# Kernel tuning notes

Measured on AMD Instinct MI355X. Metric: run time of the kernel, lower is better.

The kernel has to match this reference:

```python
import jax, jax.numpy as jnp
import numpy as np

B, O, R = 4, 1000, 20000
NF, RD, ED = 6, 1, 100
RH, OH = 150, 100


def setup_inputs() -> dict:
    key = jax.random.key(0)
    ks = jax.random.split(key, 20)
    s = 0.05
    inp = {
        "objects": jax.random.normal(ks[0], (B, O, NF), jnp.float32),
        "sender_relations": jax.random.uniform(ks[1], (B, O, R), jnp.float32),
        "receiver_relations": jax.random.uniform(ks[2], (B, O, R), jnp.float32),
        "relation_info": jax.random.normal(ks[3], (B, R, RD), jnp.float32),
        # relational MLP: (2*NF+RD) -> 150 -> 150 -> 150 -> ED, ReLU after every layer
        "rw1": jax.random.normal(ks[4], (2 * NF + RD, RH), jnp.float32) * s,
        "rb1": jnp.zeros((RH,), jnp.float32),
        "rw2": jax.random.normal(ks[5], (RH, RH), jnp.float32) * s,
        "rb2": jnp.zeros((RH,), jnp.float32),
        "rw3": jax.random.normal(ks[6], (RH, RH), jnp.float32) * s,
        "rb3": jnp.zeros((RH,), jnp.float32),
        "rw4": jax.random.normal(ks[7], (RH, ED), jnp.float32) * s,
        "rb4": jnp.zeros((ED,), jnp.float32),
        # object MLP: (NF+ED) -> 100 -> 2, ReLU only after first layer
        "ow1": jax.random.normal(ks[8], (NF + ED, OH), jnp.float32) * s,
        "ob1": jnp.zeros((OH,), jnp.float32),
        "ow2": jax.random.normal(ks[9], (OH, 2), jnp.float32) * s,
        "ob2": jnp.zeros((2,), jnp.float32),
    }
    return inp


def reference(objects, sender_relations, receiver_relations, relation_info,
              rw1, rb1, rw2, rb2, rw3, rb3, rw4, rb4,
              ow1, ob1, ow2, ob2):
    # marshalling: dense one-hot gather via bmm
    senders = jnp.einsum('bnr,bnf->brf', sender_relations, objects)    # [B,R,NF]
    receivers = jnp.einsum('bnr,bnf->brf', receiver_relations, objects)  # [B,R,NF]
    Bm = jnp.concatenate([senders, receivers, relation_info], axis=2)  # [B,R,2NF+RD]
    # relational MLP (ReLU after every layer, including the last)
    h = jax.nn.relu(Bm @ rw1 + rb1)
    h = jax.nn.relu(h @ rw2 + rb2)
    h = jax.nn.relu(h @ rw3 + rb3)
    E = jax.nn.relu(h @ rw4 + rb4)                                     # [B,R,ED]
    # aggregator: dense scatter via bmm
    effect_receivers = jnp.einsum('bnr,brf->bnf', receiver_relations, E)  # [B,O,ED]
    C = jnp.concatenate([objects, effect_receivers], axis=2)           # [B,O,NF+ED]
    # object MLP, flattened over batch*objects like the torch view(-1, input)
    Cf = C.reshape(-1, C.shape[-1])
    o = jax.nn.relu(Cf @ ow1 + ob1)
    return o @ ow2 + ob2                                               # [B*O, 2]
```

## Files before the change

kernel.cpp:

```cpp
#include <hip/hip_runtime.h>

#define B_   4
#define O_   1000
#define R_   20000
#define NF_  6
#define EDP_ 128
#define KS_  25
#define CHUNK_ 800
#define MPAD_ 1024

#define ET_OFF   2560000
#define PART_OFF 7680000
#define WT_USHORTS (4 * 2 * 25600)

typedef short bf16x8 __attribute__((ext_vector_type(8)));
typedef float f32x4  __attribute__((ext_vector_type(4)));
typedef unsigned short ushort4v __attribute__((ext_vector_type(4)));
typedef unsigned short ushort8v __attribute__((ext_vector_type(8)));

#define MFMA16 __builtin_amdgcn_mfma_f32_16x16x32_bf16

__device__ __forceinline__ unsigned short f2bf(float x) {
    union { float f; unsigned int u; } v; v.f = x;
    unsigned int r = (v.u + 0x7FFFu + ((v.u >> 16) & 1u)) >> 16;
    return (unsigned short)r;
}

__device__ __forceinline__ float bf2f(unsigned short h) {
    union { unsigned int u; float f; } v; v.u = (unsigned int)h << 16;
    return v.f;
}

__global__ __launch_bounds__(256) void k_prep(
    const float* __restrict__ rw1, const float* __restrict__ rb1,
    const float* __restrict__ rw2, const float* __restrict__ rb2,
    const float* __restrict__ rw3, const float* __restrict__ rb3,
    const float* __restrict__ rw4, const float* __restrict__ rb4,
    unsigned short* __restrict__ Wt, float* __restrict__ bfp)
{
    const int l = blockIdx.y;
    const float* Ws[4] = {rw1, rw2, rw3, rw4};
    const float* Bs[4] = {rb1, rb2, rb3, rb4};
    const int   Ksz[4] = {13, 150, 150, 150};
    const int   Nsz[4] = {150, 150, 150, 100};
    const float* w = Ws[l];
    const int K = Ksz[l], N = Nsz[l];

    int idx = blockIdx.x * 256 + threadIdx.x;
    if (idx < 25600) {
        int n = idx / 160, k = idx % 160;
        float v = (k < K && n < N) ? w[k * N + n] : 0.f;
        unsigned short h = f2bf(v);
        unsigned short lo = f2bf(v - bf2f(h));
        Wt[(size_t)l * 51200 + idx]         = h;
        Wt[(size_t)l * 51200 + 25600 + idx] = lo;
    }
    if (blockIdx.x == 0 && threadIdx.x < 160)
        bfp[l * 160 + threadIdx.x] = (threadIdx.x < (unsigned)N) ? Bs[l][threadIdx.x] : 0.f;
}

__global__ __launch_bounds__(256) void k_marshal(
    const float* __restrict__ obj, const float* __restrict__ S,
    const float* __restrict__ RRm, const float* __restrict__ rinfo,
    float* __restrict__ bmp)
{
    __shared__ float sobj[500 * NF_];
    const int b = blockIdx.y, z = blockIdx.z;
    const int n0 = z * 500;
    for (int i = threadIdx.x; i < 500 * NF_; i += 256)
        sobj[i] = obj[(size_t)b * O_ * NF_ + (size_t)n0 * NF_ + i];
    __syncthreads();

    const int r = blockIdx.x * 256 + threadIdx.x;
    if (r >= R_) return;

    const size_t base = (size_t)b * O_ * R_ + (size_t)n0 * R_ + r;
    const float* Sp = S + base;
    const float* Rp = RRm + base;

    float ss[NF_] = {0.f, 0.f, 0.f, 0.f, 0.f, 0.f};
    float rs[NF_] = {0.f, 0.f, 0.f, 0.f, 0.f, 0.f};

    #pragma unroll 4
    for (int n = 0; n < 500; ++n) {
        float sv = Sp[(size_t)n * R_];
        float rv = Rp[(size_t)n * R_];
        #pragma unroll
        for (int f = 0; f < NF_; ++f) {
            float o = sobj[n * NF_ + f];
            ss[f] = fmaf(sv, o, ss[f]);
            rs[f] = fmaf(rv, o, rs[f]);
        }
    }

    float* outp = bmp + ((size_t)z * 80000 + (size_t)b * R_ + r) * 16;
    #pragma unroll
    for (int f = 0; f < NF_; ++f) {
        outp[f]     = ss[f];
        outp[6 + f] = rs[f];
    }
    outp[12] = (z == 0) ? rinfo[(size_t)b * R_ + r] : 0.f;
}

template<int NT>
__device__ __forceinline__ void layer_mm2(
    const unsigned short (*act)[168],
    const unsigned short* __restrict__ Wh, const unsigned short* __restrict__ Wl,
    int arow0, int koff, int cl, f32x4 (*acc)[10])
{
    #pragma unroll
    for (int m = 0; m < 2; ++m)
        #pragma unroll
        for (int n = 0; n < NT; ++n) acc[m][n] = (f32x4){0.f, 0.f, 0.f, 0.f};
    #pragma unroll
    for (int ks = 0; ks < 5; ++ks) {
        bf16x8 a0 = *(const bf16x8*)&act[arow0][ks * 32 + koff];
        bf16x8 a1 = *(const bf16x8*)&act[arow0 + 16][ks * 32 + koff];
        #pragma unroll
        for (int n = 0; n < NT; ++n) {
            bf16x8 wh = *(const bf16x8*)(Wh + (size_t)(n * 16 + cl) * 160 + ks * 32 + koff);
            bf16x8 wl = *(const bf16x8*)(Wl + (size_t)(n * 16 + cl) * 160 + ks * 32 + koff);
            acc[0][n] = MFMA16(a0, wh, acc[0][n], 0, 0, 0);
            acc[0][n] = MFMA16(a0, wl, acc[0][n], 0, 0, 0);
            acc[1][n] = MFMA16(a1, wh, acc[1][n], 0, 0, 0);
            acc[1][n] = MFMA16(a1, wl, acc[1][n], 0, 0, 0);
        }
    }
}

template<int NT>
__device__ __forceinline__ void epi2(
    f32x4 (*acc)[10], const float* __restrict__ bias,
    unsigned short (*out)[168], int m0, int cl, int rg0)
{
    __syncthreads();
    #pragma unroll
    for (int m = 0; m < 2; ++m) {
        #pragma unroll
        for (int n = 0; n < NT; ++n) {
            int col = n * 16 + cl;
            float bv = bias[col];
            #pragma unroll
            for (int rg = 0; rg < 4; ++rg) {
                float v = fmaxf(acc[m][n][rg] + bv, 0.f);
                out[m0 + m * 16 + rg0 + rg][col] = f2bf(v);
            }
        }
    }
    __syncthreads();
}

__global__ __launch_bounds__(256) void k_mlp(
    const float* __restrict__ bmp, unsigned short* __restrict__ Et,
    const unsigned short* __restrict__ Wt, const float* __restrict__ bfp)
{
    __shared__ unsigned short act[128][168];
    __shared__ unsigned short alo[128][32];
    const int t = threadIdx.x;
    const size_t row0 = (size_t)blockIdx.x * 128;

    for (int idx = t; idx < 128 * 32; idx += 256) {
        int rr = idx >> 5, k = idx & 31;
        float v = 0.f;
        if (k < 13)
            v = bmp[(row0 + rr) * 16 + k]
              + bmp[(size_t)80000 * 16 + (row0 + rr) * 16 + k];
        unsigned short h = f2bf(v);
        act[rr][k] = h;
        alo[rr][k] = f2bf(v - bf2f(h));
    }
    __syncthreads();

    const int lane = t & 63, wave = t >> 6;
    const int m0    = wave * 32;
    const int arow0 = m0 + (lane & 15);
    const int koff  = (lane >> 4) * 8;
    const int cl    = lane & 15;
    const int rg0   = (lane >> 4) * 4;

    f32x4 acc[2][10];

    {
        const unsigned short* Wh = Wt;
        const unsigned short* Wl = Wt + 25600;
        bf16x8 ah0 = *(const bf16x8*)&act[arow0][koff];
        bf16x8 al0 = *(const bf16x8*)&alo[arow0][koff];
        bf16x8 ah1 = *(const bf16x8*)&act[arow0 + 16][koff];
        bf16x8 al1 = *(const bf16x8*)&alo[arow0 + 16][koff];
        #pragma unroll
        for (int n = 0; n < 10; ++n) {
            bf16x8 wh = *(const bf16x8*)(Wh + (size_t)(n * 16 + cl) * 160 + koff);
            bf16x8 wl = *(const bf16x8*)(Wl + (size_t)(n * 16 + cl) * 160 + koff);
            f32x4 a = (f32x4){0.f, 0.f, 0.f, 0.f};
            a = MFMA16(ah0, wh, a, 0, 0, 0);
            a = MFMA16(ah0, wl, a, 0, 0, 0);
            a = MFMA16(al0, wh, a, 0, 0, 0);
            acc[0][n] = a;
            f32x4 c = (f32x4){0.f, 0.f, 0.f, 0.f};
            c = MFMA16(ah1, wh, c, 0, 0, 0);
            c = MFMA16(ah1, wl, c, 0, 0, 0);
            c = MFMA16(al1, wh, c, 0, 0, 0);
            acc[1][n] = c;
        }
    }
    epi2<10>(acc, bfp + 0 * 160, act, m0, cl, rg0);

    layer_mm2<10>(act, Wt + 1 * 51200, Wt + 1 * 51200 + 25600, arow0, koff, cl, acc);
    epi2<10>(acc, bfp + 1 * 160, act, m0, cl, rg0);

    layer_mm2<10>(act, Wt + 2 * 51200, Wt + 2 * 51200 + 25600, arow0, koff, cl, acc);
    epi2<10>(acc, bfp + 2 * 160, act, m0, cl, rg0);

    layer_mm2<7>(act, Wt + 3 * 51200, Wt + 3 * 51200 + 25600, arow0, koff, cl, acc);
    epi2<7>(acc, bfp + 3 * 160, act, m0, cl, rg0);

    for (int idx = t; idx < 128 * 128; idx += 256) {
        int rr = idx & 127, j = idx >> 7;
        size_t gr = row0 + rr;
        int b = (int)(gr / R_);
        int r = (int)(gr - (size_t)b * R_);
        Et[((size_t)(b * EDP_ + j)) * R_ + r] = (j < 100) ? act[rr][j] : (unsigned short)0;
    }
}

__global__ __launch_bounds__(256) void k_agg(
    const float* __restrict__ RRm, const unsigned short* __restrict__ Et,
    float* __restrict__ part)
{
    __shared__ unsigned short sB[2][128][36];
    const int t = threadIdx.x;
    const int mt = blockIdx.x, b = blockIdx.y, kz = blockIdx.z;
    const int lane = t & 63, wave = t >> 6;
    const int k0 = kz * CHUNK_;

    const int br0 = t >> 2, bc0 = (t & 3) * 8;
    const int br1 = br0 + 64;
    const unsigned short* EtB = Et + (size_t)b * EDP_ * R_;

    const int cl = lane & 15, koff = (lane >> 4) * 8;
    int n0 = mt * 128 + wave * 32 + cl;
    int n1 = n0 + 16;
    if (n0 > 999) n0 = 999;
    if (n1 > 999) n1 = 999;
    const float* Ap0 = RRm + ((size_t)(b * O_) + n0) * R_ + k0 + koff;
    const float* Ap1 = RRm + ((size_t)(b * O_) + n1) * R_ + k0 + koff;

    f32x4 acc[2][8] = {};
    float4 a0c, a1c, a2c, a3c;
    float4 a0n = {0,0,0,0}, a1n = {0,0,0,0}, a2n = {0,0,0,0}, a3n = {0,0,0,0};

    {
        ushort8v v0 = *(const ushort8v*)(EtB + (size_t)br0 * R_ + k0 + bc0);
        ushort8v v1 = *(const ushort8v*)(EtB + (size_t)br1 * R_ + k0 + bc0);
        *(ushort8v*)&sB[0][br0][bc0] = v0;
        *(ushort8v*)&sB[0][br1][bc0] = v1;
        a0c = *(const float4*)(Ap0 + 0);
        a1c = *(const float4*)(Ap0 + 4);
        a2c = *(const float4*)(Ap1 + 0);
        a3c = *(const float4*)(Ap1 + 4);
    }
    __syncthreads();

    for (int it = 0; it < CHUNK_ / 32; ++it) {
        const int cur = it & 1, nxt = cur ^ 1;
        const bool more = (it + 1 < CHUNK_ / 32);
        ushort8v v0, v1;
        if (more) {
            const int kb = k0 + (it + 1) * 32;
            v0 = *(const ushort8v*)(EtB + (size_t)br0 * R_ + kb + bc0);
            v1 = *(const ushort8v*)(EtB + (size_t)br1 * R_ + kb + bc0);
            a0n = *(const float4*)(Ap0 + (it + 1) * 32);
            a1n = *(const float4*)(Ap0 + (it + 1) * 32 + 4);
            a2n = *(const float4*)(Ap1 + (it + 1) * 32);
            a3n = *(const float4*)(Ap1 + (it + 1) * 32 + 4);
        }
        bf16x8 af0, af1;
        af0[0] = (short)f2bf(a0c.x); af0[1] = (short)f2bf(a0c.y);
        af0[2] = (short)f2bf(a0c.z); af0[3] = (short)f2bf(a0c.w);
        af0[4] = (short)f2bf(a1c.x); af0[5] = (short)f2bf(a1c.y);
        af0[6] = (short)f2bf(a1c.z); af0[7] = (short)f2bf(a1c.w);
        af1[0] = (short)f2bf(a2c.x); af1[1] = (short)f2bf(a2c.y);
        af1[2] = (short)f2bf(a2c.z); af1[3] = (short)f2bf(a2c.w);
        af1[4] = (short)f2bf(a3c.x); af1[5] = (short)f2bf(a3c.y);
        af1[6] = (short)f2bf(a3c.z); af1[7] = (short)f2bf(a3c.w);
        #pragma unroll
        for (int ni = 0; ni < 8; ++ni) {
            bf16x8 bf = *(const bf16x8*)&sB[cur][ni * 16 + cl][koff];
            acc[0][ni] = MFMA16(af0, bf, acc[0][ni], 0, 0, 0);
            acc[1][ni] = MFMA16(af1, bf, acc[1][ni], 0, 0, 0);
        }
        if (more) {
            *(ushort8v*)&sB[nxt][br0][bc0] = v0;
            *(ushort8v*)&sB[nxt][br1][bc0] = v1;
        }
        __syncthreads();
        a0c = a0n; a1c = a1n; a2c = a2n; a3c = a3n;
    }

    float* pp = part + ((size_t)(kz * 4 + b) * MPAD_) * 128;
    #pragma unroll
    for (int mg = 0; mg < 2; ++mg) {
        const int rowb = mt * 128 + wave * 32 + mg * 16 + (lane >> 4) * 4;
        #pragma unroll
        for (int ni = 0; ni < 8; ++ni)
            #pragma unroll
            for (int rg = 0; rg < 4; ++rg)
                pp[(size_t)(rowb + rg) * 128 + ni * 16 + cl] = acc[mg][ni][rg];
    }
}

__global__ __launch_bounds__(256) void k_obj(
    const float* __restrict__ obj, const float* __restrict__ part,
    const float* __restrict__ ow1, const float* __restrict__ ob1,
    const float* __restrict__ ow2, const float* __restrict__ ob2,
    float* __restrict__ out)
{
    __shared__ float C[8][112];
    __shared__ float h[8][104];
    const int t = threadIdx.x;
    const int g0 = blockIdx.x * 8;

    for (int idx = t; idx < 8 * NF_; idx += 256) {
        int rr = idx / NF_, f = idx % NF_;
        C[rr][f] = obj[(size_t)(g0 + rr) * NF_ + f];
    }
    for (int idx = t; idx < 8 * 100; idx += 256) {
        int rr = idx / 100, f = idx % 100;
        int g = g0 + rr, b = g / 1000, n = g % 1000;
        float s = 0.f;
        for (int z = 0; z < KS_; ++z)
            s += part[((size_t)(z * 4 + b) * MPAD_ + n) * 128 + f];
        C[rr][6 + f] = s;
    }
    __syncthreads();

    for (int idx = t; idx < 8 * 100; idx += 256) {
        int rr = idx / 100, j = idx % 100;
        float acc = ob1[j];
        for (int k = 0; k < 106; ++k)
            acc = fmaf(C[rr][k], ow1[k * 100 + j], acc);
        h[rr][j] = fmaxf(acc, 0.f);
    }
    __syncthreads();

    if (t < 16) {
        int rr = t >> 1, j = t & 1;
        float acc = ob2[j];
        for (int k = 0; k < 100; ++k)
            acc = fmaf(h[rr][k], ow2[k * 2 + j], acc);
        out[(size_t)(g0 + rr) * 2 + j] = acc;
    }
}

extern "C" void kernel_launch(void* const* d_in, const int* in_sizes, int n_in,
                              void* d_out, int out_size, void* d_ws, size_t ws_size,
                              hipStream_t stream)
{
    const float* obj   = (const float*)d_in[0];
    const float* S     = (const float*)d_in[1];
    const float* RRm   = (const float*)d_in[2];
    const float* rinfo = (const float*)d_in[3];
    const float* rw1   = (const float*)d_in[4];
    const float* rb1   = (const float*)d_in[5];
    const float* rw2   = (const float*)d_in[6];
    const float* rb2   = (const float*)d_in[7];
    const float* rw3   = (const float*)d_in[8];
    const float* rb3   = (const float*)d_in[9];
    const float* rw4   = (const float*)d_in[10];
    const float* rb4   = (const float*)d_in[11];
    const float* ow1   = (const float*)d_in[12];
    const float* ob1   = (const float*)d_in[13];
    const float* ow2   = (const float*)d_in[14];
    const float* ob2   = (const float*)d_in[15];

    float* ws            = (float*)d_ws;
    float* bmp           = ws;
    unsigned short* Et   = (unsigned short*)(ws + ET_OFF);
    float* part          = ws + PART_OFF;
    unsigned short* Wt   = (unsigned short*)(ws + PART_OFF);
    float* bfp           = ws + PART_OFF + (WT_USHORTS / 2);
    float* out           = (float*)d_out;

    k_prep<<<dim3(100, 4), 256, 0, stream>>>(rw1, rb1, rw2, rb2, rw3, rb3, rw4, rb4,
                                             Wt, bfp);
    k_marshal<<<dim3(79, 4, 2), 256, 0, stream>>>(obj, S, RRm, rinfo, bmp);
    k_mlp<<<dim3(625), 256, 0, stream>>>(bmp, Et, Wt, bfp);
    k_agg<<<dim3(8, 4, KS_), 256, 0, stream>>>(RRm, Et, part);
    k_obj<<<dim3(500), 256, 0, stream>>>(obj, part, ow1, ob1, ow2, ob2, out);
}
```

Baseline: 419.1 us.

## Split MLP block tile across waves in N dimension, halve rows per block

The relational MLP kernel now processes 64 rows per block instead of 128, with the four waves arranged 2x2 so each wave computes half of the output columns for 32 rows. This halves per-wave accumulator registers and LDS per block, and doubles the grid to 1250 blocks, aiming for higher occupancy and better load balance. The cost is twice the weight traffic per row processed and extra barriers, since waves now share activation rows between layers.

```diff
diff --git a/kernel.cpp b/kernel.cpp
--- a/kernel.cpp
+++ b/kernel.cpp
@@ -103,63 +103,62 @@
 }
 
 template<int NT>
-__device__ __forceinline__ void layer_mm2(
+__device__ __forceinline__ void layer_mmW(
     const unsigned short (*act)[168],
     const unsigned short* __restrict__ Wh, const unsigned short* __restrict__ Wl,
-    int arow0, int koff, int cl, f32x4 (*acc)[10])
+    int arow0, int koff, int cl, int nb, f32x4 (*acc)[5])
 {
     #pragma unroll
     for (int m = 0; m < 2; ++m)
         #pragma unroll
-        for (int n = 0; n < NT; ++n) acc[m][n] = (f32x4){0.f, 0.f, 0.f, 0.f};
+        for (int j = 0; j < NT; ++j) acc[m][j] = (f32x4){0.f, 0.f, 0.f, 0.f};
     #pragma unroll
     for (int ks = 0; ks < 5; ++ks) {
         bf16x8 a0 = *(const bf16x8*)&act[arow0][ks * 32 + koff];
         bf16x8 a1 = *(const bf16x8*)&act[arow0 + 16][ks * 32 + koff];
         #pragma unroll
-        for (int n = 0; n < NT; ++n) {
-            bf16x8 wh = *(const bf16x8*)(Wh + (size_t)(n * 16 + cl) * 160 + ks * 32 + koff);
-            bf16x8 wl = *(const bf16x8*)(Wl + (size_t)(n * 16 + cl) * 160 + ks * 32 + koff);
-            acc[0][n] = MFMA16(a0, wh, acc[0][n], 0, 0, 0);
-            acc[0][n] = MFMA16(a0, wl, acc[0][n], 0, 0, 0);
-            acc[1][n] = MFMA16(a1, wh, acc[1][n], 0, 0, 0);
-            acc[1][n] = MFMA16(a1, wl, acc[1][n], 0, 0, 0);
+        for (int j = 0; j < NT; ++j) {
+            const size_t wo = (size_t)((nb + j) * 16 + cl) * 160 + ks * 32 + koff;
+            bf16x8 wh = *(const bf16x8*)(Wh + wo);
+            bf16x8 wl = *(const bf16x8*)(Wl + wo);
+            acc[0][j] = MFMA16(a0, wh, acc[0][j], 0, 0, 0);
+            acc[0][j] = MFMA16(a0, wl, acc[0][j], 0, 0, 0);
+            acc[1][j] = MFMA16(a1, wh, acc[1][j], 0, 0, 0);
+            acc[1][j] = MFMA16(a1, wl, acc[1][j], 0, 0, 0);
         }
     }
 }
 
 template<int NT>
-__device__ __forceinline__ void epi2(
-    f32x4 (*acc)[10], const float* __restrict__ bias,
-    unsigned short (*out)[168], int m0, int cl, int rg0)
-{
-    __syncthreads();
+__device__ __forceinline__ void epiW(
+    f32x4 (*acc)[5], const float* __restrict__ bias,
+    unsigned short (*out)[168], int m0, int cl, int rg0, int nb)
+{
     #pragma unroll
     for (int m = 0; m < 2; ++m) {
         #pragma unroll
-        for (int n = 0; n < NT; ++n) {
-            int col = n * 16 + cl;
+        for (int j = 0; j < NT; ++j) {
+            int col = (nb + j) * 16 + cl;
             float bv = bias[col];
             #pragma unroll
             for (int rg = 0; rg < 4; ++rg) {
-                float v = fmaxf(acc[m][n][rg] + bv, 0.f);
+                float v = fmaxf(acc[m][j][rg] + bv, 0.f);
                 out[m0 + m * 16 + rg0 + rg][col] = f2bf(v);
             }
         }
     }
-    __syncthreads();
 }
 
 __global__ __launch_bounds__(256) void k_mlp(
     const float* __restrict__ bmp, unsigned short* __restrict__ Et,
     const unsigned short* __restrict__ Wt, const float* __restrict__ bfp)
 {
-    __shared__ unsigned short act[128][168];
-    __shared__ unsigned short alo[128][32];
+    __shared__ unsigned short act[64][168];
+    __shared__ unsigned short alo[64][32];
     const int t = threadIdx.x;
-    const size_t row0 = (size_t)blockIdx.x * 128;
-
-    for (int idx = t; idx < 128 * 32; idx += 256) {
+    const size_t row0 = (size_t)blockIdx.x * 64;
+
+    for (int idx = t; idx < 64 * 32; idx += 256) {
         int rr = idx >> 5, k = idx & 31;
         float v = 0.f;
         if (k < 13)
@@ -172,13 +171,14 @@
     __syncthreads();
 
     const int lane = t & 63, wave = t >> 6;
-    const int m0    = wave * 32;
+    const int wm = wave >> 1, wn = wave & 1;
+    const int m0    = wm * 32;
     const int arow0 = m0 + (lane & 15);
     const int koff  = (lane >> 4) * 8;
     const int cl    = lane & 15;
     const int rg0   = (lane >> 4) * 4;
 
-    f32x4 acc[2][10];
+    f32x4 acc[2][5];
 
     {
         const unsigned short* Wh = Wt;
@@ -188,34 +188,49 @@
         bf16x8 ah1 = *(const bf16x8*)&act[arow0 + 16][koff];
         bf16x8 al1 = *(const bf16x8*)&alo[arow0 + 16][koff];
         #pragma unroll
-        for (int n = 0; n < 10; ++n) {
-            bf16x8 wh = *(const bf16x8*)(Wh + (size_t)(n * 16 + cl) * 160 + koff);
-            bf16x8 wl = *(const bf16x8*)(Wl + (size_t)(n * 16 + cl) * 160 + koff);
+        for (int j = 0; j < 5; ++j) {
+            const size_t wo = (size_t)((wn * 5 + j) * 16 + cl) * 160 + koff;
+            bf16x8 wh = *(const bf16x8*)(Wh + wo);
+            bf16x8 wl = *(const bf16x8*)(Wl + wo);
             f32x4 a = (f32x4){0.f, 0.f, 0.f, 0.f};
             a = MFMA16(ah0, wh, a, 0, 0, 0);
             a = MFMA16(ah0, wl, a, 0, 0, 0);
             a = MFMA16(al0, wh, a, 0, 0, 0);
-            acc[0][n] = a;
+            acc[0][j] = a;
             f32x4 c = (f32x4){0.f, 0.f, 0.f, 0.f};
             c = MFMA16(ah1, wh, c, 0, 0, 0);
             c = MFMA16(ah1, wl, c, 0, 0, 0);
             c = MFMA16(al1, wh, c, 0, 0, 0);
-            acc[1][n] = c;
-        }
-    }
-    epi2<10>(acc, bfp + 0 * 160, act, m0, cl, rg0);
-
-    layer_mm2<10>(act, Wt + 1 * 51200, Wt + 1 * 51200 + 25600, arow0, koff, cl, acc);
-    epi2<10>(acc, bfp + 1 * 160, act, m0, cl, rg0);
-
-    layer_mm2<10>(act, Wt + 2 * 51200, Wt + 2 * 51200 + 25600, arow0, koff, cl, acc);
-    epi2<10>(acc, bfp + 2 * 160, act, m0, cl, rg0);
-
-    layer_mm2<7>(act, Wt + 3 * 51200, Wt + 3 * 51200 + 25600, arow0, koff, cl, acc);
-    epi2<7>(acc, bfp + 3 * 160, act, m0, cl, rg0);
-
-    for (int idx = t; idx < 128 * 128; idx += 256) {
-        int rr = idx & 127, j = idx >> 7;
+            acc[1][j] = c;
+        }
+    }
+    __syncthreads();
+    epiW<5>(acc, bfp + 0 * 160, act, m0, cl, rg0, wn * 5);
+    __syncthreads();
+
+    layer_mmW<5>(act, Wt + 1 * 51200, Wt + 1 * 51200 + 25600, arow0, koff, cl, wn * 5, acc);
+    __syncthreads();
+    epiW<5>(acc, bfp + 1 * 160, act, m0, cl, rg0, wn * 5);
+    __syncthreads();
+
+    layer_mmW<5>(act, Wt + 2 * 51200, Wt + 2 * 51200 + 25600, arow0, koff, cl, wn * 5, acc);
+    __syncthreads();
+    epiW<5>(acc, bfp + 2 * 160, act, m0, cl, rg0, wn * 5);
+    __syncthreads();
+
+    if (wn == 0)
+        layer_mmW<4>(act, Wt + 3 * 51200, Wt + 3 * 51200 + 25600, arow0, koff, cl, 0, acc);
+    else
+        layer_mmW<3>(act, Wt + 3 * 51200, Wt + 3 * 51200 + 25600, arow0, koff, cl, 4, acc);
+    __syncthreads();
+    if (wn == 0)
+        epiW<4>(acc, bfp + 3 * 160, act, m0, cl, rg0, 0);
+    else
+        epiW<3>(acc, bfp + 3 * 160, act, m0, cl, rg0, 4);
+    __syncthreads();
+
+    for (int idx = t; idx < 64 * 128; idx += 256) {
+        int rr = idx & 63, j = idx >> 6;
         size_t gr = row0 + rr;
         int b = (int)(gr / R_);
         int r = (int)(gr - (size_t)b * R_);
@@ -384,7 +399,7 @@
     k_prep<<<dim3(100, 4), 256, 0, stream>>>(rw1, rb1, rw2, rb2, rw3, rb3, rw4, rb4,
                                              Wt, bfp);
     k_marshal<<<dim3(79, 4, 2), 256, 0, stream>>>(obj, S, RRm, rinfo, bmp);
-    k_mlp<<<dim3(625), 256, 0, stream>>>(bmp, Et, Wt, bfp);
+    k_mlp<<<dim3(1250), 256, 0, stream>>>(bmp, Et, Wt, bfp);
     k_agg<<<dim3(8, 4, KS_), 256, 0, stream>>>(RRm, Et, part);
     k_obj<<<dim3(500), 256, 0, stream>>>(obj, part, ow1, ob1, ow2, ob2, out);
 }
```

After: 354.6 us. 15.4% less time.
